# Optimization experiments

Hardware: AMD Instinct MI355X
Metric: run time of the kernel (lower is better)

The kernel has to match this reference:

```python
import jax, jax.numpy as jnp
import numpy as np

N = 8192      # nodes (= hidden_channels / heads)
E = 262144    # edges (avg degree 32)
IN = 256      # in_channels
H = 8         # heads
C = 32        # out_channels per head
NEG_SLOPE = 0.2


def setup_inputs() -> dict:
    key = jax.random.key(0)
    ks = jax.random.split(key, 8)
    x = jax.random.normal(ks[0], (N, IN), jnp.float32)
    edge_index = jax.random.randint(ks[1], (2, E), 0, N, dtype=jnp.int32)
    lin_w = jax.random.normal(ks[2], (H * C, IN), jnp.float32) * (1.0 / np.sqrt(IN))
    att_src = jax.random.normal(ks[3], (H, C), jnp.float32) * 0.1
    att_dst = jax.random.normal(ks[4], (H, C), jnp.float32) * 0.1
    bias = jax.random.normal(ks[5], (H * C,), jnp.float32) * 0.01
    out_w = jax.random.normal(ks[6], (C, N * H * C), jnp.float32) * (1.0 / np.sqrt(N * H * C))
    out_b = jax.random.normal(ks[7], (C,), jnp.float32) * 0.01
    return {"x": x, "edge_index": edge_index, "lin_w": lin_w, "att_src": att_src,
            "att_dst": att_dst, "bias": bias, "out_w": out_w, "out_b": out_b}


def reference(x, edge_index, lin_w, att_src, att_dst, bias, out_w, out_b):
    n = x.shape[0]
    # PyG GATConv default: add self loops
    loop = jnp.arange(n, dtype=edge_index.dtype)
    src = jnp.concatenate([edge_index[0], loop])  # message sources j
    dst = jnp.concatenate([edge_index[1], loop])  # message targets i
    # per-head linear projection: [n, H, C]
    xh = (x @ lin_w.T).reshape(n, H, C)
    a_src = jnp.einsum('nhc,hc->nh', xh, att_src)  # [n, H]
    a_dst = jnp.einsum('nhc,hc->nh', xh, att_dst)  # [n, H]
    # edge attention logits + segment softmax over incoming edges of each dst
    e = jax.nn.leaky_relu(a_src[src] + a_dst[dst], negative_slope=NEG_SLOPE)  # [E', H]
    m = jax.ops.segment_max(e, dst, num_segments=n)        # [n, H]
    ex = jnp.exp(e - m[dst])
    denom = jax.ops.segment_sum(ex, dst, num_segments=n)   # [n, H]
    alpha = ex / denom[dst]                                 # [E', H]
    # weighted scatter-add aggregation
    agg = jax.ops.segment_sum(alpha[:, :, None] * xh[src], dst, num_segments=n)  # [n, H, C]
    out = agg.reshape(n, H * C) + bias
    # flatten all nodes, dense output layer, softmax
    y = out.reshape(-1) @ out_w.T + out_b  # [C]
    return jax.nn.softmax(y)
```

## Files before the change

### kernel.cpp

```cpp
#include <hip/hip_runtime.h>


namespace {
constexpr int  kN    = 8192;
constexpr int  kE    = 262144;
constexpr int  kTotE = kE + kN;
constexpr long kK    = 2097152;
constexpr int  kNBF  = 1024;
constexpr int  kChunk = (int)(kK / kNBF);
}

__global__ __launch_bounds__(256) void gemm_xh(const float* __restrict__ x,
                                               const float* __restrict__ lw,
                                               float* __restrict__ xh) {
  __shared__ float As[16][68];
  __shared__ float Bs[16][68];
  const int t  = threadIdx.x;
  const int tx = t & 15, ty = t >> 4;
  const int rowBase = blockIdx.x * 64;
  const int colBase = blockIdx.y * 64;
  const int lr = t >> 2;
  const int lk = (t & 3) * 4;

  float acc[4][4] = {};
  for (int kc = 0; kc < 256; kc += 16) {
    float4 av = *(const float4*)(x  + (long)(rowBase + lr) * 256 + kc + lk);
    float4 bv = *(const float4*)(lw + (long)(colBase + lr) * 256 + kc + lk);
    __syncthreads();
    As[lk + 0][lr] = av.x; As[lk + 1][lr] = av.y; As[lk + 2][lr] = av.z; As[lk + 3][lr] = av.w;
    Bs[lk + 0][lr] = bv.x; Bs[lk + 1][lr] = bv.y; Bs[lk + 2][lr] = bv.z; Bs[lk + 3][lr] = bv.w;
    __syncthreads();
#pragma unroll
    for (int k = 0; k < 16; k++) {
      float4 a4 = *(const float4*)(&As[k][ty * 4]);
      float4 b4 = *(const float4*)(&Bs[k][tx * 4]);
      float aa[4] = {a4.x, a4.y, a4.z, a4.w};
      float bb[4] = {b4.x, b4.y, b4.z, b4.w};
#pragma unroll
      for (int i = 0; i < 4; i++)
#pragma unroll
        for (int j = 0; j < 4; j++) acc[i][j] += aa[i] * bb[j];
    }
  }
#pragma unroll
  for (int i = 0; i < 4; i++) {
    float4 o = make_float4(acc[i][0], acc[i][1], acc[i][2], acc[i][3]);
    *(float4*)(xh + (long)(rowBase + ty * 4 + i) * 256 + colBase + tx * 4) = o;
  }
}

__global__ __launch_bounds__(256) void att_cnt(const float* __restrict__ xh,
                                               const float* __restrict__ att_s,
                                               const float* __restrict__ att_d,
                                               float* __restrict__ a_src,
                                               float* __restrict__ a_dst,
                                               int* __restrict__ cnt) {
  const int n = blockIdx.x, t = threadIdx.x;
  float v = xh[(long)n * 256 + t];
  float s = v * att_s[t];
  float d = v * att_d[t];
#pragma unroll
  for (int off = 16; off; off >>= 1) {
    s += __shfl_down(s, off, 32);
    d += __shfl_down(d, off, 32);
  }
  if ((t & 31) == 0) {
    a_src[n * 8 + (t >> 5)] = s;
    a_dst[n * 8 + (t >> 5)] = d;
  }
  if (t == 0) cnt[n] = 1;
}

__global__ __launch_bounds__(256) void degree(const int* __restrict__ ei, int* __restrict__ cnt) {
  int idx = blockIdx.x * 256 + threadIdx.x;
  if (idx < kE) atomicAdd(&cnt[ei[kE + idx]], 1);
}

__global__ __launch_bounds__(1024) void scan_cnt(const int* __restrict__ cnt,
                                                 int* __restrict__ rowptr,
                                                 int* __restrict__ wpos) {
  __shared__ int s[1024];
  const int t = threadIdx.x;
  int v[8]; int sum = 0;
#pragma unroll
  for (int q = 0; q < 8; q++) { v[q] = cnt[t * 8 + q]; sum += v[q]; }
  s[t] = sum;
  __syncthreads();
  for (int off = 1; off < 1024; off <<= 1) {
    int add = (t >= off) ? s[t - off] : 0;
    __syncthreads();
    s[t] += add;
    __syncthreads();
  }
  int excl = s[t] - sum;
#pragma unroll
  for (int q = 0; q < 8; q++) {
    rowptr[t * 8 + q] = excl;
    wpos[t * 8 + q]   = excl;
    excl += v[q];
  }
  if (t == 1023) rowptr[kN] = s[1023];
}

__global__ __launch_bounds__(256) void scatter_csr(const int* __restrict__ ei,
                                                   int* __restrict__ wpos,
                                                   int* __restrict__ csr) {
  int idx = blockIdx.x * 256 + threadIdx.x;
  if (idx >= kTotE) return;
  int s, d;
  if (idx < kE) { s = ei[idx]; d = ei[kE + idx]; }
  else          { s = idx - kE; d = s; }
  int pos = atomicAdd(&wpos[d], 1);
  csr[pos] = s;
}

__global__ __launch_bounds__(256) void agg_kernel(const float* __restrict__ xh,
                                                  const float* __restrict__ a_src,
                                                  const float* __restrict__ a_dst,
                                                  const int* __restrict__ rowptr,
                                                  const int* __restrict__ csr,
                                                  const float* __restrict__ bias,
                                                  float* __restrict__ out_flat) {
  const int i = blockIdx.x, t = threadIdx.x, h = t >> 5;
  const float ad = a_dst[i * 8 + h];
  const int beg = rowptr[i], end = rowptr[i + 1];
  float acc = 0.f, den = 0.f;
  for (int j = beg; j < end; j++) {
    int s = csr[j];
    float e = a_src[s * 8 + h] + ad;
    e = (e > 0.f) ? e : 0.2f * e;
    float w = __expf(e);
    den += w;
    acc += w * xh[(long)s * 256 + t];
  }
  out_flat[(long)i * 256 + t] = acc / den + bias[t];
}

__global__ __launch_bounds__(256) void final_dot(const float* __restrict__ of,
                                                 const float* __restrict__ w,
                                                 float* __restrict__ part) {
  const int t = threadIdx.x, b = blockIdx.x;
  float acc[32];
#pragma unroll
  for (int c = 0; c < 32; c++) acc[c] = 0.f;
#pragma unroll
  for (int it = 0; it < kChunk / 1024; it++) {
    const long k = (long)b * kChunk + it * 1024 + t * 4;
    float4 f = *(const float4*)(of + k);
#pragma unroll
    for (int c = 0; c < 32; c++) {
      float4 wv = *(const float4*)(w + (long)c * kK + k);
      acc[c] += wv.x * f.x + wv.y * f.y + wv.z * f.z + wv.w * f.w;
    }
  }
#pragma unroll
  for (int c = 0; c < 32; c++) {
    float v = acc[c];
    v += __shfl_down(v, 32, 64);
    v += __shfl_down(v, 16, 64);
    v += __shfl_down(v, 8, 64);
    v += __shfl_down(v, 4, 64);
    v += __shfl_down(v, 2, 64);
    v += __shfl_down(v, 1, 64);
    acc[c] = v;
  }
  __shared__ float s[4][32];
  const int lane = t & 63, wid = t >> 6;
  if (lane == 0) {
#pragma unroll
    for (int c = 0; c < 32; c++) s[wid][c] = acc[c];
  }
  __syncthreads();
  if (t < 32) part[b * 32 + t] = s[0][t] + s[1][t] + s[2][t] + s[3][t];
}

__global__ __launch_bounds__(1024) void finalize(const float* __restrict__ part,
                                                 const float* __restrict__ ob,
                                                 float* __restrict__ out) {
  __shared__ float s[32][33];
  const int t = threadIdx.x;
  const int c = t & 31, r = t >> 5;
  float sum = 0.f;
  for (int i = r; i < kNBF; i += 32) sum += part[i * 32 + c];
  s[c][r] = sum;
  __syncthreads();
  if (t < 32) {
    float y = ob[t];
#pragma unroll
    for (int r2 = 0; r2 < 32; r2++) y += s[t][r2];
    float m = y;
#pragma unroll
    for (int off = 16; off; off >>= 1) m = fmaxf(m, __shfl_xor(m, off, 32));
    float e = __expf(y - m);
    float d = e;
#pragma unroll
    for (int off = 16; off; off >>= 1) d += __shfl_xor(d, off, 32);
    out[t] = e / d;
  }
}

extern "C" void kernel_launch(void* const* d_in, const int* in_sizes, int n_in,
                              void* d_out, int out_size, void* d_ws, size_t ws_size,
                              hipStream_t stream) {
  (void)in_sizes; (void)n_in; (void)out_size; (void)ws_size;
  const float* x     = (const float*)d_in[0];
  const int*   ei    = (const int*)  d_in[1];
  const float* lin_w = (const float*)d_in[2];
  const float* att_s = (const float*)d_in[3];
  const float* att_d = (const float*)d_in[4];
  const float* bias  = (const float*)d_in[5];
  const float* out_w = (const float*)d_in[6];
  const float* out_b = (const float*)d_in[7];
  float* out = (float*)d_out;

  float* xh       = (float*)d_ws;
  float* out_flat = xh + kK;
  float* a_src    = out_flat + kK;
  float* a_dst    = a_src + kN * 8;
  float* part     = a_dst + kN * 8;
  int*   cnt      = (int*)(part + kNBF * 32);
  int*   rowptr   = cnt + kN;
  int*   wpos     = rowptr + (kN + 1);
  int*   csr      = wpos + kN;

  gemm_xh   <<<dim3(128, 4), 256, 0, stream>>>(x, lin_w, xh);
  att_cnt   <<<kN, 256, 0, stream>>>(xh, att_s, att_d, a_src, a_dst, cnt);
  degree    <<<kE / 256, 256, 0, stream>>>(ei, cnt);
  scan_cnt  <<<1, 1024, 0, stream>>>(cnt, rowptr, wpos);
  scatter_csr<<<kTotE / 256, 256, 0, stream>>>(ei, wpos, csr);
  agg_kernel<<<kN, 256, 0, stream>>>(xh, a_src, a_dst, rowptr, csr, bias, out_flat);
  final_dot <<<kNBF, 256, 0, stream>>>(out_flat, out_w, part);
  finalize  <<<1, 1024, 0, stream>>>(part, out_b, out);
}
```

Before: 497.8 us.

## Precompute edge attention weights during CSR scatter, unroll aggregation, widen final dot

Edge attention weights (leaky-relu and exp for all 8 heads) are now computed once per edge inside the CSR scatter kernel and stored in CSR order, so the aggregation kernel only loads a precomputed weight. This avoids each of the 32 threads per head redundantly gathering a_src and computing exp. The aggregation loop is unrolled by 4 to keep more independent gathers in flight, and the final dot product uses 2048 blocks each handling a single chunk. In exchange it adds an 8.4 MB weight buffer that is written and then re-read.

Result: no change. 493.8 us (-0.8%).

```diff
diff --git a/kernel.cpp b/kernel.cpp
--- a/kernel.cpp
+++ b/kernel.cpp
@@ -6,8 +6,7 @@
 constexpr int  kE    = 262144;
 constexpr int  kTotE = kE + kN;
 constexpr long kK    = 2097152;
-constexpr int  kNBF  = 1024;
-constexpr int  kChunk = (int)(kK / kNBF);
+constexpr int  kNBF  = 2048;
 }
 
 __global__ __launch_bounds__(256) void gemm_xh(const float* __restrict__ x,
@@ -103,8 +102,11 @@
 }
 
 __global__ __launch_bounds__(256) void scatter_csr(const int* __restrict__ ei,
+                                                   const float* __restrict__ a_src,
+                                                   const float* __restrict__ a_dst,
                                                    int* __restrict__ wpos,
-                                                   int* __restrict__ csr) {
+                                                   int* __restrict__ csr,
+                                                   float* __restrict__ w8) {
   int idx = blockIdx.x * 256 + threadIdx.x;
   if (idx >= kTotE) return;
   int s, d;
@@ -112,24 +114,52 @@
   else          { s = idx - kE; d = s; }
   int pos = atomicAdd(&wpos[d], 1);
   csr[pos] = s;
+  float4 s0 = *(const float4*)(a_src + s * 8);
+  float4 s1 = *(const float4*)(a_src + s * 8 + 4);
+  float4 d0 = *(const float4*)(a_dst + d * 8);
+  float4 d1 = *(const float4*)(a_dst + d * 8 + 4);
+  float e[8] = {s0.x + d0.x, s0.y + d0.y, s0.z + d0.z, s0.w + d0.w,
+                s1.x + d1.x, s1.y + d1.y, s1.z + d1.z, s1.w + d1.w};
+  float w[8];
+#pragma unroll
+  for (int h = 0; h < 8; h++) {
+    float ee = (e[h] > 0.f) ? e[h] : 0.2f * e[h];
+    w[h] = __expf(ee);
+  }
+  float4* wp = (float4*)(w8 + (long)pos * 8);
+  wp[0] = make_float4(w[0], w[1], w[2], w[3]);
+  wp[1] = make_float4(w[4], w[5], w[6], w[7]);
 }
 
 __global__ __launch_bounds__(256) void agg_kernel(const float* __restrict__ xh,
-                                                  const float* __restrict__ a_src,
-                                                  const float* __restrict__ a_dst,
+                                                  const float* __restrict__ w8,
                                                   const int* __restrict__ rowptr,
                                                   const int* __restrict__ csr,
                                                   const float* __restrict__ bias,
                                                   float* __restrict__ out_flat) {
   const int i = blockIdx.x, t = threadIdx.x, h = t >> 5;
-  const float ad = a_dst[i * 8 + h];
   const int beg = rowptr[i], end = rowptr[i + 1];
   float acc = 0.f, den = 0.f;
-  for (int j = beg; j < end; j++) {
+  int j = beg;
+  for (; j + 4 <= end; j += 4) {
+    int s0 = csr[j], s1 = csr[j + 1], s2 = csr[j + 2], s3 = csr[j + 3];
+    float w0 = w8[(long)(j + 0) * 8 + h];
+    float w1 = w8[(long)(j + 1) * 8 + h];
+    float w2 = w8[(long)(j + 2) * 8 + h];
+    float w3 = w8[(long)(j + 3) * 8 + h];
+    float f0 = xh[(long)s0 * 256 + t];
+    float f1 = xh[(long)s1 * 256 + t];
+    float f2 = xh[(long)s2 * 256 + t];
+    float f3 = xh[(long)s3 * 256 + t];
+    den += (w0 + w1) + (w2 + w3);
+    acc += w0 * f0;
+    acc += w1 * f1;
+    acc += w2 * f2;
+    acc += w3 * f3;
+  }
+  for (; j < end; j++) {
     int s = csr[j];
-    float e = a_src[s * 8 + h] + ad;
-    e = (e > 0.f) ? e : 0.2f * e;
-    float w = __expf(e);
+    float w = w8[(long)j * 8 + h];
     den += w;
     acc += w * xh[(long)s * 256 + t];
   }
@@ -140,18 +170,13 @@
                                                  const float* __restrict__ w,
                                                  float* __restrict__ part) {
   const int t = threadIdx.x, b = blockIdx.x;
+  const long k = (long)b * 1024 + t * 4;
+  float4 f = *(const float4*)(of + k);
   float acc[32];
 #pragma unroll
-  for (int c = 0; c < 32; c++) acc[c] = 0.f;
-#pragma unroll
-  for (int it = 0; it < kChunk / 1024; it++) {
-    const long k = (long)b * kChunk + it * 1024 + t * 4;
-    float4 f = *(const float4*)(of + k);
-#pragma unroll
-    for (int c = 0; c < 32; c++) {
-      float4 wv = *(const float4*)(w + (long)c * kK + k);
-      acc[c] += wv.x * f.x + wv.y * f.y + wv.z * f.z + wv.w * f.w;
-    }
+  for (int c = 0; c < 32; c++) {
+    float4 wv = *(const float4*)(w + (long)c * kK + k);
+    acc[c] = wv.x * f.x + wv.y * f.y + wv.z * f.z + wv.w * f.w;
   }
 #pragma unroll
   for (int c = 0; c < 32; c++) {
@@ -218,17 +243,18 @@
   float* a_src    = out_flat + kK;
   float* a_dst    = a_src + kN * 8;
   float* part     = a_dst + kN * 8;
-  int*   cnt      = (int*)(part + kNBF * 32);
+  float* w8       = part + (long)kNBF * 32;
+  int*   cnt      = (int*)(w8 + (long)kTotE * 8);
   int*   rowptr   = cnt + kN;
   int*   wpos     = rowptr + (kN + 1);
   int*   csr      = wpos + kN;
 
-  gemm_xh   <<<dim3(128, 4), 256, 0, stream>>>(x, lin_w, xh);
-  att_cnt   <<<kN, 256, 0, stream>>>(xh, att_s, att_d, a_src, a_dst, cnt);
-  degree    <<<kE / 256, 256, 0, stream>>>(ei, cnt);
-  scan_cnt  <<<1, 1024, 0, stream>>>(cnt, rowptr, wpos);
-  scatter_csr<<<kTotE / 256, 256, 0, stream>>>(ei, wpos, csr);
-  agg_kernel<<<kN, 256, 0, stream>>>(xh, a_src, a_dst, rowptr, csr, bias, out_flat);
-  final_dot <<<kNBF, 256, 0, stream>>>(out_flat, out_w, part);
-  finalize  <<<1, 1024, 0, stream>>>(part, out_b, out);
-}
+  gemm_xh    <<<dim3(128, 4), 256, 0, stream>>>(x, lin_w, xh);
+  att_cnt    <<<kN, 256, 0, stream>>>(xh, att_s, att_d, a_src, a_dst, cnt);
+  degree     <<<kE / 256, 256, 0, stream>>>(ei, cnt);
+  scan_cnt   <<<1, 1024, 0, stream>>>(cnt, rowptr, wpos);
+  scatter_csr<<<(kTotE + 255) / 256, 256, 0, stream>>>(ei, a_src, a_dst, wpos, csr, w8);
+  agg_kernel <<<kN, 256, 0, stream>>>(xh, w8, rowptr, csr, bias, out_flat);
+  final_dot  <<<kNBF, 256, 0, stream>>>(out_flat, out_w, part);
+  finalize   <<<1, 1024, 0, stream>>>(part, out_b, out);
+}
```
